# Performance work log

Measured on AMD Instinct MI355X. Metric: run time of the kernel, lower is better.

The kernel has to match this reference:

```python
import jax, jax.numpy as jnp
import numpy as np

MAX_TRAV = 21  # matches the torch module constant


def setup_inputs() -> dict:
    key = jax.random.key(0)
    k1, _ = jax.random.split(key)
    B, H, W = 4, 2048, 2048
    untraversable = jax.random.randint(k1, (B, H, W), 0, 2).astype(jnp.bool_)
    max_sq = jnp.ones((1,), dtype=jnp.float32) * float(MAX_TRAV ** 2)  # 441.0
    return {"untraversable": untraversable, "max_sq": max_sq}


def _chamfer(untraversable, max_sq):
    big = max_sq[0]
    B, H, W = untraversable.shape
    # 0 at obstacles, MAX_TRAV^2 elsewhere (values are small exact ints in fp32)
    sq = jnp.where(untraversable, jnp.float32(0.0), big)
    # odd increments 1,3,...,41: cumulative sum of first k odds = k^2
    ds = jnp.arange(1, 2 * MAX_TRAV + 1, 2, dtype=jnp.float32)

    col = jnp.full((B, H, 1), big, dtype=jnp.float32)

    def hstep(s, d):
        from_right = jnp.concatenate([s[:, :, 1:] + d, col], axis=2)
        from_left = jnp.concatenate([col, s[:, :, :-1] + d], axis=2)
        return jnp.minimum(s, jnp.minimum(from_right, from_left)), None

    sq, _ = jax.lax.scan(hstep, sq, ds)

    row = jnp.full((B, 1, W), big, dtype=jnp.float32)

    def vstep(s, d):
        from_below = jnp.concatenate([s[:, 1:, :] + d, row], axis=1)
        from_above = jnp.concatenate([row, s[:, :-1, :] + d], axis=1)
        return jnp.minimum(s, jnp.minimum(from_below, from_above)), None

    sq, _ = jax.lax.scan(vstep, sq, ds)
    return jnp.sqrt(sq)


def reference(untraversable, max_sq):
    return _chamfer(untraversable, max_sq)
```

## Files before the change

### kernel.cpp

```cpp
#include <hip/hip_runtime.h>
#include <cstdint>

#define BB 4
#define HH 2048
#define WW 2048
#define MAXT 21
#define BIGSQ 441
#define SEN (1u << 6)

typedef float floatx4 __attribute__((ext_vector_type(4)));
typedef unsigned short u16x2 __attribute__((ext_vector_type(2)));

static __device__ __forceinline__ uint32_t umax32(uint32_t a, uint32_t b) { return a > b ? a : b; }
static __device__ __forceinline__ int imin(int a, int b) { return a < b ? a : b; }

__global__ __launch_bounds__(256) void hpass(const int* __restrict__ in,
                                             uint8_t* __restrict__ dh) {
    const int tid  = threadIdx.x;
    const int lane = tid & 63;
    const int w    = tid >> 6;
    const int row  = (blockIdx.x << 2) + w;
    const int ro   = row * WW;
    const int* rp  = in + ro;
    const int li   = 63 - lane;

    uint4 q[8];
    #pragma unroll
    for (int j = 0; j < 8; ++j)
        q[j] = *(const uint4*)(rp + (j << 8) + (lane << 2));

    unsigned long long Bc[4], Bn[4], rbc[4], rbp[4];
    #pragma unroll
    for (int k = 0; k < 4; ++k) rbp[k] = 0;
    Bc[0] = __ballot(q[0].x != 0);
    Bc[1] = __ballot(q[0].y != 0);
    Bc[2] = __ballot(q[0].z != 0);
    Bc[3] = __ballot(q[0].w != 0);
    #pragma unroll
    for (int k = 0; k < 4; ++k) rbc[k] = __brevll(Bc[k]);

    #pragma unroll
    for (int j = 0; j < 8; ++j) {
        if (j < 7) {
            Bn[0] = __ballot(q[j + 1].x != 0);
            Bn[1] = __ballot(q[j + 1].y != 0);
            Bn[2] = __ballot(q[j + 1].z != 0);
            Bn[3] = __ballot(q[j + 1].w != 0);
        } else {
            Bn[0] = Bn[1] = Bn[2] = Bn[3] = 0;
        }

        int a[4], b[4], c[4], e[4];
        #pragma unroll
        for (int k = 0; k < 4; ++k) {
            unsigned long long S  = (Bc[k] >> lane) | ((Bn[k] << 1) << li);
            unsigned long long SL = (rbc[k] >> li)  | ((rbp[k] << 1) << lane);
            uint32_t s  = (uint32_t)S;
            uint32_t sl = (uint32_t)SL;
            a[k] = 4 * __builtin_ctz(s | SEN) + k;
            b[k] = 4 * __builtin_ctz((s >> 1) | SEN) + 4 + k;
            c[k] = 4 * __builtin_ctz(sl | SEN) - k;
            e[k] = 4 * __builtin_ctz((sl >> 1) | SEN) + 4 - k;
        }
        const int A3 = a[3], A2 = imin(a[2], A3), A1 = imin(a[1], A2), A0 = imin(a[0], A1);
        const int B0 = b[0], B1 = imin(B0, b[1]), B2 = imin(B1, b[2]);
        const int C0 = c[0], C1 = imin(C0, c[1]), C2 = imin(C1, c[2]), C3 = imin(C2, c[3]);
        const int E3 = e[3], E2 = imin(e[2], E3), E1 = imin(e[1], E2);

        int d0 = imin(imin(A0,               imin(C0, E1)    ), MAXT);
        int d1 = imin(imin(imin(A1, B0) - 1, imin(C1, E2) + 1), MAXT);
        int d2 = imin(imin(imin(A2, B1) - 2, imin(C2, E3) + 2), MAXT);
        int d3 = imin(imin(imin(A3, B2) - 3, C3 + 3          ), MAXT);

        uint32_t pk = (uint32_t)d0 | ((uint32_t)d1 << 8) | ((uint32_t)d2 << 16) | ((uint32_t)d3 << 24);
        *(uint32_t*)(dh + ro + (j << 8) + (lane << 2)) = pk;

        #pragma unroll
        for (int k = 0; k < 4; ++k) {
            rbp[k] = rbc[k];
            Bc[k]  = Bn[k];
            rbc[k] = __brevll(Bn[k]);
        }
    }
}

__global__ __launch_bounds__(256) void vpass(const uint8_t* __restrict__ dh,
                                             float* __restrict__ out) {
    __shared__ uint16_t s[106][128];
    const int tid = threadIdx.x;
    const int bid = blockIdx.x;
    const int swz = (bid & 7) * 256 + (bid >> 3);
    const int x0  = (swz & 15) << 7;
    const int y0  = ((swz >> 4) & 31) << 6;
    const int b   = swz >> 9;
    const int base = b * (HH * WW);

    for (int i = tid; i < 106 * 8; i += 256) {
        const int r   = i >> 3;
        const int c16 = (i & 7) << 4;
        const int gy  = y0 - 21 + r;
        uint4 pk0, pk1;
        if (gy >= 0 && gy < HH) {
            const uint8_t* p = dh + base + gy * WW + x0 + c16;
            uint4 u = *(const uint4*)p;
            #pragma unroll
            for (int h = 0; h < 4; ++h) {
                uint32_t word = (&u.x)[h];
                uint32_t e0 = word & 0xff, e1 = (word >> 8) & 0xff;
                uint32_t e2 = (word >> 16) & 0xff, e3 = word >> 24;
                uint32_t lo = (e0 * e0) | ((e1 * e1) << 16);
                uint32_t hi = (e2 * e2) | ((e3 * e3) << 16);
                if (h < 2) { (&pk0.x)[h * 2] = lo; (&pk0.x)[h * 2 + 1] = hi; }
                else       { (&pk1.x)[(h - 2) * 2] = lo; (&pk1.x)[(h - 2) * 2 + 1] = hi; }
            }
        } else {
            pk0.x = pk0.y = pk0.z = pk0.w = BIGSQ | (BIGSQ << 16);
            pk1 = pk0;
        }
        *(uint4*)&s[r][c16]     = pk0;
        *(uint4*)&s[r][c16 + 8] = pk1;
    }
    __syncthreads();

    const int lane = tid & 63;
    const int w    = tid >> 6;
    const int cg   = (lane & 31) << 2;
    const int rofs = lane >> 5;
    for (int k = 0; k < 8; ++k) {
        const int j  = (w << 4) + (k << 1) + rofs;
        const int yl = 21 + j;

        uint2 q = *(const uint2*)&s[yl][cg];
        u16x2 V0 = __builtin_bit_cast(u16x2, q.x);
        u16x2 V1 = __builtin_bit_cast(u16x2, q.y);

        for (int d = 1; d <= MAXT; ++d) {
            const uint32_t dd = (uint32_t)(d * d);
            u16x2 M = __builtin_elementwise_max(V0, V1);
            uint32_t m32 = __builtin_bit_cast(uint32_t, M);
            uint32_t h = umax32(m32 & 0xffffu, m32 >> 16);
            if (__all(dd >= h)) break;
            uint2 a  = *(const uint2*)&s[yl - d][cg];
            uint2 bq = *(const uint2*)&s[yl + d][cg];
            u16x2 D  = { (unsigned short)dd, (unsigned short)dd };
            u16x2 A0 = __builtin_bit_cast(u16x2, a.x),  A1 = __builtin_bit_cast(u16x2, a.y);
            u16x2 B0 = __builtin_bit_cast(u16x2, bq.x), B1 = __builtin_bit_cast(u16x2, bq.y);
            V0 = __builtin_elementwise_min(V0, (u16x2)(__builtin_elementwise_min(A0, B0) + D));
            V1 = __builtin_elementwise_min(V1, (u16x2)(__builtin_elementwise_min(A1, B1) + D));
        }

        const uint32_t r0 = __builtin_bit_cast(uint32_t, V0);
        const uint32_t r1 = __builtin_bit_cast(uint32_t, V1);
        floatx4 o;
        o.x = sqrtf((float)(r0 & 0xffffu));
        o.y = sqrtf((float)(r0 >> 16));
        o.z = sqrtf((float)(r1 & 0xffffu));
        o.w = sqrtf((float)(r1 >> 16));
        floatx4* op = (floatx4*)&out[base + (y0 + j) * WW + x0 + cg];
        __builtin_nontemporal_store(o, op);
    }
}

extern "C" void kernel_launch(void* const* d_in, const int* in_sizes, int n_in,
                              void* d_out, int out_size, void* d_ws, size_t ws_size,
                              hipStream_t stream) {
    const int* unt = (const int*)d_in[0];
    uint8_t* dh    = (uint8_t*)d_ws;
    float* out     = (float*)d_out;

    hpass<<<dim3(BB * HH / 4), 256, 0, stream>>>(unt, dh);
    vpass<<<dim3(WW / 128 * HH / 64 * BB), 256, 0, stream>>>(dh, out);
}
```

Measured before the change: 37.92 us.

## Fuse horizontal and vertical passes into one cooperative kernel with grid sync

Merges the two kernel launches into a single cooperative kernel of 1024 persistent blocks. Each block first runs the horizontal pass over 8 rows, then a grid-wide sync, then the vertical pass over 2 tiles. This is meant to remove the second launch and the gap between kernels. In exchange it adds grid-sync overhead, caps the grid at a fixed number of resident blocks, and halves the parallel slack in the vertical phase.

After: 143.7 us. 279% more time.

```diff
diff --git a/kernel.cpp b/kernel.cpp
--- a/kernel.cpp
+++ b/kernel.cpp
@@ -1,5 +1,8 @@
 #include <hip/hip_runtime.h>
+#include <hip/hip_cooperative_groups.h>
 #include <cstdint>
+
+namespace coop = cooperative_groups;
 
 #define BB 4
 #define HH 2048
@@ -14,15 +17,10 @@
 static __device__ __forceinline__ uint32_t umax32(uint32_t a, uint32_t b) { return a > b ? a : b; }
 static __device__ __forceinline__ int imin(int a, int b) { return a < b ? a : b; }
 
-__global__ __launch_bounds__(256) void hpass(const int* __restrict__ in,
-                                             uint8_t* __restrict__ dh) {
-    const int tid  = threadIdx.x;
-    const int lane = tid & 63;
-    const int w    = tid >> 6;
-    const int row  = (blockIdx.x << 2) + w;
-    const int ro   = row * WW;
-    const int* rp  = in + ro;
-    const int li   = 63 - lane;
+static __device__ __forceinline__ void hrow(const int* __restrict__ rp,
+                                            uint8_t* __restrict__ dst,
+                                            const int lane) {
+    const int li = 63 - lane;
 
     uint4 q[8];
     #pragma unroll
@@ -73,7 +71,7 @@
         int d3 = imin(imin(imin(A3, B2) - 3, C3 + 3          ), MAXT);
 
         uint32_t pk = (uint32_t)d0 | ((uint32_t)d1 << 8) | ((uint32_t)d2 << 16) | ((uint32_t)d3 << 24);
-        *(uint32_t*)(dh + ro + (j << 8) + (lane << 2)) = pk;
+        *(uint32_t*)(dst + (j << 8) + (lane << 2)) = pk;
 
         #pragma unroll
         for (int k = 0; k < 4; ++k) {
@@ -84,80 +82,97 @@
     }
 }
 
-__global__ __launch_bounds__(256) void vpass(const uint8_t* __restrict__ dh,
-                                             float* __restrict__ out) {
+__global__ __launch_bounds__(256, 4) void fused_coop(const int* __restrict__ in,
+                                                     uint8_t* __restrict__ dh,
+                                                     float* __restrict__ out) {
     __shared__ uint16_t s[106][128];
-    const int tid = threadIdx.x;
-    const int bid = blockIdx.x;
-    const int swz = (bid & 7) * 256 + (bid >> 3);
-    const int x0  = (swz & 15) << 7;
-    const int y0  = ((swz >> 4) & 31) << 6;
-    const int b   = swz >> 9;
-    const int base = b * (HH * WW);
-
-    for (int i = tid; i < 106 * 8; i += 256) {
-        const int r   = i >> 3;
-        const int c16 = (i & 7) << 4;
-        const int gy  = y0 - 21 + r;
-        uint4 pk0, pk1;
-        if (gy >= 0 && gy < HH) {
-            const uint8_t* p = dh + base + gy * WW + x0 + c16;
-            uint4 u = *(const uint4*)p;
-            #pragma unroll
-            for (int h = 0; h < 4; ++h) {
-                uint32_t word = (&u.x)[h];
-                uint32_t e0 = word & 0xff, e1 = (word >> 8) & 0xff;
-                uint32_t e2 = (word >> 16) & 0xff, e3 = word >> 24;
-                uint32_t lo = (e0 * e0) | ((e1 * e1) << 16);
-                uint32_t hi = (e2 * e2) | ((e3 * e3) << 16);
-                if (h < 2) { (&pk0.x)[h * 2] = lo; (&pk0.x)[h * 2 + 1] = hi; }
-                else       { (&pk1.x)[(h - 2) * 2] = lo; (&pk1.x)[(h - 2) * 2 + 1] = hi; }
-            }
-        } else {
-            pk0.x = pk0.y = pk0.z = pk0.w = BIGSQ | (BIGSQ << 16);
-            pk1 = pk0;
-        }
-        *(uint4*)&s[r][c16]     = pk0;
-        *(uint4*)&s[r][c16 + 8] = pk1;
-    }
-    __syncthreads();
-
+    const int tid  = threadIdx.x;
     const int lane = tid & 63;
     const int w    = tid >> 6;
-    const int cg   = (lane & 31) << 2;
-    const int rofs = lane >> 5;
-    for (int k = 0; k < 8; ++k) {
-        const int j  = (w << 4) + (k << 1) + rofs;
-        const int yl = 21 + j;
+    const int bid  = blockIdx.x;
+    const int si   = (bid & 7) * 128 + (bid >> 3);
 
-        uint2 q = *(const uint2*)&s[yl][cg];
-        u16x2 V0 = __builtin_bit_cast(u16x2, q.x);
-        u16x2 V1 = __builtin_bit_cast(u16x2, q.y);
+    #pragma unroll
+    for (int rr = 0; rr < 2; ++rr) {
+        const int row = (si << 3) + (w << 1) + rr;
+        const int ro  = row * WW;
+        hrow(in + ro, dh + ro, lane);
+    }
 
-        for (int d = 1; d <= MAXT; ++d) {
-            const uint32_t dd = (uint32_t)(d * d);
-            u16x2 M = __builtin_elementwise_max(V0, V1);
-            uint32_t m32 = __builtin_bit_cast(uint32_t, M);
-            uint32_t h = umax32(m32 & 0xffffu, m32 >> 16);
-            if (__all(dd >= h)) break;
-            uint2 a  = *(const uint2*)&s[yl - d][cg];
-            uint2 bq = *(const uint2*)&s[yl + d][cg];
-            u16x2 D  = { (unsigned short)dd, (unsigned short)dd };
-            u16x2 A0 = __builtin_bit_cast(u16x2, a.x),  A1 = __builtin_bit_cast(u16x2, a.y);
-            u16x2 B0 = __builtin_bit_cast(u16x2, bq.x), B1 = __builtin_bit_cast(u16x2, bq.y);
-            V0 = __builtin_elementwise_min(V0, (u16x2)(__builtin_elementwise_min(A0, B0) + D));
-            V1 = __builtin_elementwise_min(V1, (u16x2)(__builtin_elementwise_min(A1, B1) + D));
+    coop::this_grid().sync();
+
+    for (int qq = 0; qq < 2; ++qq) {
+        const int ti = (si << 1) + qq;
+        const int xt = ti & 15;
+        const int gt = ti >> 4;
+        const int b  = gt >> 5;
+        const int y0 = (gt & 31) << 6;
+        const int x0 = xt << 7;
+        const int base = b * (HH * WW);
+
+        for (int i = tid; i < 106 * 8; i += 256) {
+            const int r   = i >> 3;
+            const int c16 = (i & 7) << 4;
+            const int gy  = y0 - 21 + r;
+            uint4 pk0, pk1;
+            if (gy >= 0 && gy < HH) {
+                const uint8_t* p = dh + base + gy * WW + x0 + c16;
+                uint4 u = *(const uint4*)p;
+                #pragma unroll
+                for (int h = 0; h < 4; ++h) {
+                    uint32_t word = (&u.x)[h];
+                    uint32_t e0 = word & 0xff, e1 = (word >> 8) & 0xff;
+                    uint32_t e2 = (word >> 16) & 0xff, e3 = word >> 24;
+                    uint32_t lo = (e0 * e0) | ((e1 * e1) << 16);
+                    uint32_t hi = (e2 * e2) | ((e3 * e3) << 16);
+                    if (h < 2) { (&pk0.x)[h * 2] = lo; (&pk0.x)[h * 2 + 1] = hi; }
+                    else       { (&pk1.x)[(h - 2) * 2] = lo; (&pk1.x)[(h - 2) * 2 + 1] = hi; }
+                }
+            } else {
+                pk0.x = pk0.y = pk0.z = pk0.w = BIGSQ | (BIGSQ << 16);
+                pk1 = pk0;
+            }
+            *(uint4*)&s[r][c16]     = pk0;
+            *(uint4*)&s[r][c16 + 8] = pk1;
         }
+        __syncthreads();
 
-        const uint32_t r0 = __builtin_bit_cast(uint32_t, V0);
-        const uint32_t r1 = __builtin_bit_cast(uint32_t, V1);
-        floatx4 o;
-        o.x = sqrtf((float)(r0 & 0xffffu));
-        o.y = sqrtf((float)(r0 >> 16));
-        o.z = sqrtf((float)(r1 & 0xffffu));
-        o.w = sqrtf((float)(r1 >> 16));
-        floatx4* op = (floatx4*)&out[base + (y0 + j) * WW + x0 + cg];
-        __builtin_nontemporal_store(o, op);
+        const int cg4  = (lane & 31) << 2;
+        const int rofs = lane >> 5;
+        for (int k = 0; k < 8; ++k) {
+            const int j  = (w << 4) + (k << 1) + rofs;
+            const int yl = 21 + j;
+
+            uint2 q = *(const uint2*)&s[yl][cg4];
+            u16x2 V0 = __builtin_bit_cast(u16x2, q.x);
+            u16x2 V1 = __builtin_bit_cast(u16x2, q.y);
+
+            for (int d = 1; d <= MAXT; ++d) {
+                const uint32_t dd = (uint32_t)(d * d);
+                u16x2 M = __builtin_elementwise_max(V0, V1);
+                uint32_t m32 = __builtin_bit_cast(uint32_t, M);
+                uint32_t h = umax32(m32 & 0xffffu, m32 >> 16);
+                if (__all(dd >= h)) break;
+                uint2 a  = *(const uint2*)&s[yl - d][cg4];
+                uint2 bq = *(const uint2*)&s[yl + d][cg4];
+                u16x2 D  = { (unsigned short)dd, (unsigned short)dd };
+                u16x2 A0 = __builtin_bit_cast(u16x2, a.x),  A1 = __builtin_bit_cast(u16x2, a.y);
+                u16x2 B0 = __builtin_bit_cast(u16x2, bq.x), B1 = __builtin_bit_cast(u16x2, bq.y);
+                V0 = __builtin_elementwise_min(V0, (u16x2)(__builtin_elementwise_min(A0, B0) + D));
+                V1 = __builtin_elementwise_min(V1, (u16x2)(__builtin_elementwise_min(A1, B1) + D));
+            }
+
+            const uint32_t r0 = __builtin_bit_cast(uint32_t, V0);
+            const uint32_t r1 = __builtin_bit_cast(uint32_t, V1);
+            floatx4 o;
+            o.x = sqrtf((float)(r0 & 0xffffu));
+            o.y = sqrtf((float)(r0 >> 16));
+            o.z = sqrtf((float)(r1 & 0xffffu));
+            o.w = sqrtf((float)(r1 >> 16));
+            floatx4* op = (floatx4*)&out[base + (y0 + j) * WW + x0 + cg4];
+            __builtin_nontemporal_store(o, op);
+        }
+        __syncthreads();
     }
 }
 
@@ -166,8 +181,9 @@
                               hipStream_t stream) {
     const int* unt = (const int*)d_in[0];
     uint8_t* dh    = (uint8_t*)d_ws;
-    float* out     = (float*)d_out;
+    float* outp    = (float*)d_out;
 
-    hpass<<<dim3(BB * HH / 4), 256, 0, stream>>>(unt, dh);
-    vpass<<<dim3(WW / 128 * HH / 64 * BB), 256, 0, stream>>>(dh, out);
+    void* args[] = { (void*)&unt, (void*)&dh, (void*)&outp };
+    hipLaunchCooperativeKernel(reinterpret_cast<const void*>(fused_coop),
+                               dim3(1024), dim3(256), args, 0, stream);
 }
```
